# Kernel tuning notes

Measured on AMD Instinct MI355X. Metric: run time of the kernel, lower is better.

Reference implementation:

```python
import jax, jax.numpy as jnp
import numpy as np

B, S, D, H = 2, 2048, 1024, 16
HD = D // H

def setup_inputs() -> dict:
    key = jax.random.key(0)
    ks = jax.random.split(key, 9)
    scale = 1.0 / np.sqrt(D)
    return {
        "query": jax.random.normal(ks[0], (B, S, D), jnp.float32),
        "key":   jax.random.normal(ks[1], (B, S, D), jnp.float32),
        "value": jax.random.normal(ks[2], (B, S, D), jnp.float32),
        "Wq_w": jax.random.normal(ks[3], (D, D), jnp.float32) * scale,
        "Wq_b": jax.random.normal(ks[4], (D,), jnp.float32) * scale,
        "Wk_w": jax.random.normal(ks[5], (D, D), jnp.float32) * scale,
        "Wk_b": jax.random.normal(ks[6], (D,), jnp.float32) * scale,
        "Wv_w": jax.random.normal(ks[7], (D, D), jnp.float32) * scale,
        "Wv_b": jax.random.normal(ks[8], (D,), jnp.float32) * scale,
    }

def reference(query, key, value, Wq_w, Wq_b, Wk_w, Wk_b, Wv_w, Wv_b):
    b, s, d = query.shape
    # torch Linear: y = x @ W.T + b
    Q = query @ Wq_w.T + Wq_b
    K = key   @ Wk_w.T + Wk_b
    V = value @ Wv_w.T + Wv_b
    # [B, H, S, HD]
    Q = Q.reshape(b, -1, H, HD).transpose(0, 2, 1, 3)
    K = K.reshape(b, -1, H, HD).transpose(0, 2, 1, 3)
    V = V.reshape(b, -1, H, HD).transpose(0, 2, 1, 3)
    scores = jnp.einsum("bhqd,bhkd->bhqk", Q, K) / jnp.sqrt(jnp.float32(HD))
    attn = jax.nn.softmax(scores, axis=-1)
    context = jnp.einsum("bhqk,bhkd->bhqd", attn, V)  # [B,H,S,HD]
    attn_output = context.transpose(0, 2, 1, 3).reshape(b, -1, H * HD)  # [B,S,D]
    return (context, attn_output)
```

## Files before the change

### kernel.cpp

```cpp
#include <hip/hip_runtime.h>
#include <hip/hip_bf16.h>

constexpr int Bb = 2, Ss = 2048, Dd = 1024, Hh = 16, HD = 64;
constexpr int Mrows = Bb * Ss;
constexpr float QSCALE = 0.125f * 1.44269504088896f;
constexpr size_t CTX_ELEMS = (size_t)Bb * Hh * Ss * HD;

typedef __attribute__((ext_vector_type(8))) short   short8;
typedef __attribute__((ext_vector_type(4))) float   floatx4;
typedef __attribute__((ext_vector_type(8))) __bf16  bf16x8;

#define DEVI __device__ __forceinline__

DEVI unsigned short f2bf(float f) {
  union { float f; unsigned u; } x; x.f = f;
  return (unsigned short)((x.u + 0x7fffu + ((x.u >> 16) & 1u)) >> 16);
}
DEVI float fexp2(float x) {
#if __has_builtin(__builtin_amdgcn_exp2f)
  return __builtin_amdgcn_exp2f(x);
#else
  return __expf(x * 0.6931471805599453f);
#endif
}

constexpr size_t XE = (size_t)Mrows * Dd;
constexpr size_t WE = (size_t)Dd * Dd;
constexpr size_t OFF_W = 3 * XE;
constexpr size_t OFF_O = 3 * XE + 3 * WE;
constexpr size_t WS_NEED = (OFF_O + 3 * XE) * 2;

__global__ __launch_bounds__(256) void convert_bf16(
    const float* __restrict__ q, const float* __restrict__ k, const float* __restrict__ v,
    const float* __restrict__ wq, const float* __restrict__ wk, const float* __restrict__ wv,
    unsigned short* __restrict__ dst)
{
  const int sel = blockIdx.y;
  const float* src; size_t n, off;
  switch (sel) {
    case 0:  src = q;  n = XE; off = 0;            break;
    case 1:  src = k;  n = XE; off = XE;           break;
    case 2:  src = v;  n = XE; off = 2 * XE;       break;
    case 3:  src = wq; n = WE; off = OFF_W;        break;
    case 4:  src = wk; n = WE; off = OFF_W + WE;   break;
    default: src = wv; n = WE; off = OFF_W + 2*WE; break;
  }
  unsigned short* d = dst + off;
  const size_t stride = (size_t)gridDim.x * blockDim.x;
  for (size_t i = (size_t)blockIdx.x * blockDim.x + threadIdx.x; i < n / 8; i += stride) {
    const floatx4 a = *(const floatx4*)(src + i * 8);
    const floatx4 b = *(const floatx4*)(src + i * 8 + 4);
    short8 o;
    #pragma unroll
    for (int j = 0; j < 4; ++j) { o[j] = (short)f2bf(a[j]); o[4 + j] = (short)f2bf(b[j]); }
    *(short8*)(d + i * 8) = o;
  }
}

template<bool SWAP>
DEVI void store_out(floatx4 (&acc)[4][4], const float* __restrict__ bias,
                    unsigned short* __restrict__ out, float oscale,
                    int bm, int bn, int wm, int wn, int lrow, int lg)
{
  if constexpr (!SWAP) {
    #pragma unroll
    for (int ni = 0; ni < 4; ++ni) {
      const int gcol = bn * 128 + wn + ni * 16 + lrow;
      const float bval = bias[gcol];
      const int h = gcol >> 6, hd = gcol & 63;
      #pragma unroll
      for (int mi = 0; mi < 4; ++mi)
        #pragma unroll
        for (int r = 0; r < 4; ++r) {
          const int grow = bm * 128 + wm + mi * 16 + lg * 4 + r;
          const int b = grow >> 11, s = grow & 2047;
          out[(((size_t)(b * Hh + h) * Ss + s) << 6) + hd] = f2bf((acc[mi][ni][r] + bval) * oscale);
        }
    }
  } else {
    #pragma unroll
    for (int ni = 0; ni < 4; ++ni)
      #pragma unroll
      for (int r = 0; r < 4; ++r) {
        const int n = bn * 128 + wn + ni * 16 + lg * 4 + r;
        const float bval = bias[n];
        #pragma unroll
        for (int mi = 0; mi < 4; ++mi) {
          const int m = bm * 128 + wm + mi * 16 + lrow;
          out[(size_t)n * Mrows + m] = f2bf(acc[mi][ni][r] + bval);
        }
      }
  }
}

DEVI void gload16(const unsigned short* g, unsigned short* l) {
  __builtin_amdgcn_global_load_lds(
      (const __attribute__((address_space(1))) unsigned int*)g,
      (__attribute__((address_space(3))) unsigned int*)l, 16, 0, 0);
}

template<bool SWAP>
DEVI void gemm_core_bf16(const unsigned short* __restrict__ X,
                         const unsigned short* __restrict__ W,
                         const float* __restrict__ bias,
                         unsigned short* __restrict__ out, float oscale,
                         unsigned short* As, unsigned short* Bs, int bm, int bn)
{
  const int t = threadIdx.x, wid = t >> 6, lane = t & 63;
  const int lrow = lane & 15, lg = lane >> 4;
  const int wm = (wid >> 1) * 64, wn = (wid & 1) * 64;

  const int srow = lane >> 3;
  const int gch  = (lane & 7) ^ srow;
  const unsigned short* gA = X + (size_t)(bm * 128 + wid * 32 + srow) * Dd + gch * 8;
  const unsigned short* gB = W + (size_t)(bn * 128 + wid * 32 + srow) * Dd + gch * 8;
  unsigned short* lA = As + wid * 4 * 512;
  unsigned short* lB = Bs + wid * 4 * 512;

  floatx4 acc[4][4];
  #pragma unroll
  for (int i = 0; i < 4; ++i)
    #pragma unroll
    for (int j = 0; j < 4; ++j) acc[i][j] = 0.0f;

  for (int k0 = 0; k0 < Dd; k0 += 64) {
    __syncthreads();
    #pragma unroll
    for (int j = 0; j < 4; ++j) {
      gload16(gA + (size_t)j * 8 * Dd + k0, lA + j * 512);
      gload16(gB + (size_t)j * 8 * Dd + k0, lB + j * 512);
    }
    __syncthreads();

    #pragma unroll
    for (int kf = 0; kf < 2; ++kf) {
      bf16x8 af[4], bf[4];
      #pragma unroll
      for (int mi = 0; mi < 4; ++mi) {
        const int row = wm + mi * 16 + lrow;
        const int ch  = ((kf << 2) | lg) ^ (lrow & 7);
        af[mi] = __builtin_bit_cast(bf16x8, *(const short8*)&As[row * 64 + (ch << 3)]);
      }
      #pragma unroll
      for (int ni = 0; ni < 4; ++ni) {
        const int row = wn + ni * 16 + lrow;
        const int ch  = ((kf << 2) | lg) ^ (lrow & 7);
        bf[ni] = __builtin_bit_cast(bf16x8, *(const short8*)&Bs[row * 64 + (ch << 3)]);
      }
      #pragma unroll
      for (int mi = 0; mi < 4; ++mi)
        #pragma unroll
        for (int ni = 0; ni < 4; ++ni) {
          if constexpr (SWAP)
            acc[mi][ni] = __builtin_amdgcn_mfma_f32_16x16x32_bf16(bf[ni], af[mi], acc[mi][ni], 0, 0, 0);
          else
            acc[mi][ni] = __builtin_amdgcn_mfma_f32_16x16x32_bf16(af[mi], bf[ni], acc[mi][ni], 0, 0, 0);
        }
    }
  }
  store_out<SWAP>(acc, bias, out, oscale, bm, bn, wm, wn, lrow, lg);
}

__global__ __launch_bounds__(256, 3) void qkv_gemm_bf16(
    const unsigned short* __restrict__ ws,
    const float* __restrict__ bq, const float* __restrict__ bk, const float* __restrict__ bv,
    unsigned short* __restrict__ outbase)
{
  __shared__ __align__(16) unsigned short As[128 * 64];
  __shared__ __align__(16) unsigned short Bs[128 * 64];

  const int id  = blockIdx.y * 256 + blockIdx.x;
  const int swz = (id & 7) * 96 + (id >> 3);
  const int sel = swz >> 8;
  const int bx  = swz & 255;
  const int bm = bx >> 3, bn = bx & 7;

  const unsigned short* X = ws + (size_t)sel * XE;
  const unsigned short* W = ws + OFF_W + (size_t)sel * WE;
  const float* bias = sel == 0 ? bq : sel == 1 ? bk : bv;
  unsigned short* out = outbase + (size_t)sel * XE;

  if (sel == 2) gemm_core_bf16<true >(X, W, bias, out, 1.0f,   As, Bs, bm, bn);
  else          gemm_core_bf16<false>(X, W, bias, out, sel == 0 ? QSCALE : 1.0f, As, Bs, bm, bn);
}

constexpr int APAD = 40;

template<bool SWAP>
DEVI void gemm_core_f32(const float* __restrict__ X, const float* __restrict__ W,
                        const float* __restrict__ bias, unsigned short* __restrict__ out,
                        float oscale, unsigned short* As, unsigned short* Bs, int bm, int bn)
{
  const int t = threadIdx.x, wid = t >> 6, lane = t & 63;
  const int lrow = lane & 15, lg = lane >> 4;
  const int wm = (wid >> 1) * 64, wn = (wid & 1) * 64;

  floatx4 acc[4][4];
  #pragma unroll
  for (int i = 0; i < 4; ++i)
    #pragma unroll
    for (int j = 0; j < 4; ++j) acc[i][j] = 0.0f;

  for (int k0 = 0; k0 < Dd; k0 += 32) {
    __syncthreads();
    #pragma unroll
    for (int half = 0; half < 2; ++half) {
      const int cidx = t + half * 256;
      const int r = cidx >> 2, c = cidx & 3;
      {
        const float* ga = X + (size_t)(bm * 128 + r) * Dd + k0 + c * 8;
        const floatx4 x0 = *(const floatx4*)ga;
        const floatx4 x1 = *(const floatx4*)(ga + 4);
        short8 va;
        #pragma unroll
        for (int j = 0; j < 4; ++j) { va[j] = (short)f2bf(x0[j]); va[4+j] = (short)f2bf(x1[j]); }
        *(short8*)&As[r * APAD + c * 8] = va;
      }
      {
        const float* gb = W + (size_t)(bn * 128 + r) * Dd + k0 + c * 8;
        const floatx4 x0 = *(const floatx4*)gb;
        const floatx4 x1 = *(const floatx4*)(gb + 4);
        short8 vb;
        #pragma unroll
        for (int j = 0; j < 4; ++j) { vb[j] = (short)f2bf(x0[j]); vb[4+j] = (short)f2bf(x1[j]); }
        *(short8*)&Bs[r * APAD + c * 8] = vb;
      }
    }
    __syncthreads();

    bf16x8 af[4], bf[4];
    #pragma unroll
    for (int mi = 0; mi < 4; ++mi)
      af[mi] = __builtin_bit_cast(bf16x8, *(const short8*)&As[(wm + mi * 16 + lrow) * APAD + lg * 8]);
    #pragma unroll
    for (int ni = 0; ni < 4; ++ni)
      bf[ni] = __builtin_bit_cast(bf16x8, *(const short8*)&Bs[(wn + ni * 16 + lrow) * APAD + lg * 8]);

    #pragma unroll
    for (int mi = 0; mi < 4; ++mi)
      #pragma unroll
      for (int ni = 0; ni < 4; ++ni) {
        if constexpr (SWAP)
          acc[mi][ni] = __builtin_amdgcn_mfma_f32_16x16x32_bf16(bf[ni], af[mi], acc[mi][ni], 0, 0, 0);
        else
          acc[mi][ni] = __builtin_amdgcn_mfma_f32_16x16x32_bf16(af[mi], bf[ni], acc[mi][ni], 0, 0, 0);
      }
  }
  store_out<SWAP>(acc, bias, out, oscale, bm, bn, wm, wn, lrow, lg);
}

__global__ __launch_bounds__(256, 2) void qkv_gemm_f32(
    const float* __restrict__ q, const float* __restrict__ k, const float* __restrict__ v,
    const float* __restrict__ wq, const float* __restrict__ wk, const float* __restrict__ wv,
    const float* __restrict__ bq, const float* __restrict__ bk, const float* __restrict__ bv,
    unsigned short* __restrict__ outbase)
{
  __shared__ __align__(16) unsigned short As[128 * APAD];
  __shared__ __align__(16) unsigned short Bs[128 * APAD];

  const int id  = blockIdx.y * 256 + blockIdx.x;
  const int swz = (id & 7) * 96 + (id >> 3);
  const int sel = swz >> 8;
  const int bx  = swz & 255;
  const int bm = bx >> 3, bn = bx & 7;

  const float* X = sel == 0 ? q : sel == 1 ? k : v;
  const float* W = sel == 0 ? wq : sel == 1 ? wk : wv;
  const float* bias = sel == 0 ? bq : sel == 1 ? bk : bv;
  unsigned short* out = outbase + (size_t)sel * XE;

  if (sel == 2) gemm_core_f32<true >(X, W, bias, out, 1.0f, As, Bs, bm, bn);
  else          gemm_core_f32<false>(X, W, bias, out, sel == 0 ? QSCALE : 1.0f, As, Bs, bm, bn);
}

constexpr int KPAD  = 72;
constexpr int PWPAD = 72;

__global__ __launch_bounds__(256, 2) void attn_fwd(
    const unsigned short* __restrict__ Qw, const unsigned short* __restrict__ Kw,
    const unsigned short* __restrict__ Vw, float* __restrict__ out)
{
  __shared__ __align__(16) unsigned short Ks[2][64 * KPAD];
  __shared__ __align__(16) unsigned short Vt[2][64 * KPAD];
  __shared__ __align__(16) unsigned short Pw[4][32 * PWPAD];

  const int id  = blockIdx.y * 16 + blockIdx.x;
  const int swz = (id & 7) * 64 + (id >> 3);
  const int qb  = swz & 15, bh = swz >> 4;
  const int b   = bh >> 4, h = bh & 15;

  const int t = threadIdx.x, wid = t >> 6, lane = t & 63;
  const int lrow = lane & 15, lg = lane >> 4;
  const unsigned short* Qb = Qw + (size_t)bh * (Ss * HD);
  const unsigned short* Kb = Kw + (size_t)bh * (Ss * HD);
  const int q0 = qb * 128 + wid * 32;

  bf16x8 qf[2][2];
  #pragma unroll
  for (int qh = 0; qh < 2; ++qh)
    #pragma unroll
    for (int kf = 0; kf < 2; ++kf)
      qf[qh][kf] = __builtin_bit_cast(bf16x8,
          *(const short8*)(Qb + (size_t)(q0 + qh * 16 + lrow) * 64 + kf * 32 + lg * 8));

  floatx4 ctx[2][4];
  floatx4 l4[2];
  #pragma unroll
  for (int qh = 0; qh < 2; ++qh) {
    l4[qh] = 0.0f;
    #pragma unroll
    for (int ni = 0; ni < 4; ++ni) ctx[qh][ni] = 0.0f;
  }
  short8 ones_s;
  #pragma unroll
  for (int j = 0; j < 8; ++j) ones_s[j] = (short)0x3F80;
  const bf16x8 ones = __builtin_bit_cast(bf16x8, ones_s);

  const int sr = t >> 2, sc = t & 3;
  const unsigned short* kgp = Kb + (size_t)sr * 64;
  const unsigned short* vgp = Vw + (size_t)(h * 64 + sr) * Mrows + b * Ss;

  short8 kreg[2], vreg[2];
  auto stage_load = [&](int kv0) {
    #pragma unroll
    for (int hf = 0; hf < 2; ++hf) {
      const int c = sc + hf * 4;
      kreg[hf] = *(const short8*)(kgp + (size_t)kv0 * 64 + c * 8);
      vreg[hf] = *(const short8*)(vgp + kv0 + c * 8);
    }
  };
  auto stage_write = [&](int buf) {
    #pragma unroll
    for (int hf = 0; hf < 2; ++hf) {
      const int c = sc + hf * 4;
      *(short8*)&Ks[buf][sr * KPAD + c * 8] = kreg[hf];
      *(short8*)&Vt[buf][sr * KPAD + c * 8] = vreg[hf];
    }
  };

  stage_load(0);
  stage_write(0);
  __syncthreads();

  unsigned short* Pme = &Pw[wid][0];

  for (int it = 0; it < Ss / 64; ++it) {
    const int cur = it & 1;
    if (it + 1 < Ss / 64) stage_load((it + 1) * 64);

    floatx4 s4[2][4];
    #pragma unroll
    for (int qh = 0; qh < 2; ++qh)
      #pragma unroll
      for (int ni = 0; ni < 4; ++ni) s4[qh][ni] = 0.0f;
    #pragma unroll
    for (int ni = 0; ni < 4; ++ni)
      #pragma unroll
      for (int kf = 0; kf < 2; ++kf) {
        const bf16x8 kfrag = __builtin_bit_cast(bf16x8,
            *(const short8*)&Ks[cur][(ni * 16 + lrow) * KPAD + kf * 32 + lg * 8]);
        #pragma unroll
        for (int qh = 0; qh < 2; ++qh)
          s4[qh][ni] = __builtin_amdgcn_mfma_f32_16x16x32_bf16(qf[qh][kf], kfrag, s4[qh][ni], 0, 0, 0);
      }

    #pragma unroll
    for (int qh = 0; qh < 2; ++qh)
      #pragma unroll
      for (int ni = 0; ni < 4; ++ni)
        #pragma unroll
        for (int r = 0; r < 4; ++r) {
          const float p = fexp2(s4[qh][ni][r]);
          Pme[(qh * 16 + lg * 4 + r) * PWPAD + ni * 16 + lrow] = f2bf(p);
        }

    #pragma unroll
    for (int kvs = 0; kvs < 2; ++kvs) {
      bf16x8 pa[2];
      #pragma unroll
      for (int qh = 0; qh < 2; ++qh) {
        pa[qh] = __builtin_bit_cast(bf16x8,
            *(const short8*)&Pme[(qh * 16 + lrow) * PWPAD + kvs * 32 + lg * 8]);
        l4[qh] = __builtin_amdgcn_mfma_f32_16x16x32_bf16(pa[qh], ones, l4[qh], 0, 0, 0);
      }
      #pragma unroll
      for (int ni = 0; ni < 4; ++ni) {
        const bf16x8 vf = __builtin_bit_cast(bf16x8,
            *(const short8*)&Vt[cur][(ni * 16 + lrow) * KPAD + kvs * 32 + lg * 8]);
        #pragma unroll
        for (int qh = 0; qh < 2; ++qh)
          ctx[qh][ni] = __builtin_amdgcn_mfma_f32_16x16x32_bf16(pa[qh], vf, ctx[qh][ni], 0, 0, 0);
      }
    }

    if (it + 1 < Ss / 64) stage_write(cur ^ 1);
    __syncthreads();
  }

  #pragma unroll
  for (int qh = 0; qh < 2; ++qh) {
    floatx4 inv;
    #pragma unroll
    for (int r = 0; r < 4; ++r) inv[r] = 1.0f / l4[qh][r];
    #pragma unroll
    for (int ni = 0; ni < 4; ++ni) {
      const int hd = ni * 16 + lrow;
      #pragma unroll
      for (int r = 0; r < 4; ++r) {
        const int q = q0 + qh * 16 + lg * 4 + r;
        const float val = ctx[qh][ni][r] * inv[r];
        out[((size_t)bh * Ss + q) * 64 + hd] = val;
        out[CTX_ELEMS + (((size_t)(b * Ss + q)) << 10) + (h << 6) + hd] = val;
      }
    }
  }
}

extern "C" void kernel_launch(void* const* d_in, const int* in_sizes, int n_in,
                              void* d_out, int out_size, void* d_ws, size_t ws_size,
                              hipStream_t stream) {
  const float* q  = (const float*)d_in[0];
  const float* k  = (const float*)d_in[1];
  const float* v  = (const float*)d_in[2];
  const float* wq = (const float*)d_in[3];
  const float* bq = (const float*)d_in[4];
  const float* wk = (const float*)d_in[5];
  const float* bk = (const float*)d_in[6];
  const float* wv = (const float*)d_in[7];
  const float* bv = (const float*)d_in[8];
  unsigned short* ws = (unsigned short*)d_ws;
  float* out = (float*)d_out;

  if (ws_size >= WS_NEED) {
    convert_bf16<<<dim3(256, 6), 256, 0, stream>>>(q, k, v, wq, wk, wv, ws);
    qkv_gemm_bf16<<<dim3(256, 3), 256, 0, stream>>>(ws, bq, bk, bv, ws + OFF_O);
    attn_fwd<<<dim3(16, 32), 256, 0, stream>>>(ws + OFF_O, ws + OFF_O + XE, ws + OFF_O + 2 * XE, out);
  } else {
    qkv_gemm_f32<<<dim3(256, 3), 256, 0, stream>>>(q, k, v, wq, wk, wv, bq, bk, bv, ws);
    attn_fwd<<<dim3(16, 32), 256, 0, stream>>>(ws, ws + XE, ws + 2 * XE, out);
  }
}
```

Baseline: 105.4 us.

## Rewrite attention inner loop with 32x32 MFMA, register-resident P, direct LDS loads

```diff
diff --git a/kernel.cpp b/kernel.cpp
--- a/kernel.cpp
+++ b/kernel.cpp
@@ -6,9 +6,11 @@
 constexpr float QSCALE = 0.125f * 1.44269504088896f;
 constexpr size_t CTX_ELEMS = (size_t)Bb * Hh * Ss * HD;
 
-typedef __attribute__((ext_vector_type(8))) short   short8;
-typedef __attribute__((ext_vector_type(4))) float   floatx4;
-typedef __attribute__((ext_vector_type(8))) __bf16  bf16x8;
+typedef __attribute__((ext_vector_type(8)))  short        short8;
+typedef __attribute__((ext_vector_type(4)))  float        floatx4;
+typedef __attribute__((ext_vector_type(16))) float        floatx16;
+typedef __attribute__((ext_vector_type(4)))  unsigned int uintx4;
+typedef __attribute__((ext_vector_type(8)))  __bf16       bf16x8;
 
 #define DEVI __device__ __forceinline__
 
@@ -273,16 +275,12 @@
   else          gemm_core_f32<false>(X, W, bias, out, sel == 0 ? QSCALE : 1.0f, As, Bs, bm, bn);
 }
 
-constexpr int KPAD  = 72;
-constexpr int PWPAD = 72;
-
 __global__ __launch_bounds__(256, 2) void attn_fwd(
     const unsigned short* __restrict__ Qw, const unsigned short* __restrict__ Kw,
     const unsigned short* __restrict__ Vw, float* __restrict__ out)
 {
-  __shared__ __align__(16) unsigned short Ks[2][64 * KPAD];
-  __shared__ __align__(16) unsigned short Vt[2][64 * KPAD];
-  __shared__ __align__(16) unsigned short Pw[4][32 * PWPAD];
+  __shared__ __align__(16) unsigned short Ks[2][64 * 64];
+  __shared__ __align__(16) unsigned short Vt[2][64 * 64];
 
   const int id  = blockIdx.y * 16 + blockIdx.x;
   const int swz = (id & 7) * 64 + (id >> 3);
@@ -290,128 +288,104 @@
   const int b   = bh >> 4, h = bh & 15;
 
   const int t = threadIdx.x, wid = t >> 6, lane = t & 63;
-  const int lrow = lane & 15, lg = lane >> 4;
+  const int l31 = lane & 31, hi = lane >> 5;
   const unsigned short* Qb = Qw + (size_t)bh * (Ss * HD);
   const unsigned short* Kb = Kw + (size_t)bh * (Ss * HD);
+  const unsigned short* Vg = Vw + (size_t)(h * 64) * Mrows + b * Ss;
   const int q0 = qb * 128 + wid * 32;
 
-  bf16x8 qf[2][2];
-  #pragma unroll
-  for (int qh = 0; qh < 2; ++qh)
-    #pragma unroll
-    for (int kf = 0; kf < 2; ++kf)
-      qf[qh][kf] = __builtin_bit_cast(bf16x8,
-          *(const short8*)(Qb + (size_t)(q0 + qh * 16 + lrow) * 64 + kf * 32 + lg * 8));
-
-  floatx4 ctx[2][4];
-  floatx4 l4[2];
-  #pragma unroll
-  for (int qh = 0; qh < 2; ++qh) {
-    l4[qh] = 0.0f;
-    #pragma unroll
-    for (int ni = 0; ni < 4; ++ni) ctx[qh][ni] = 0.0f;
-  }
+  bf16x8 qf[4];
+  #pragma unroll
+  for (int hs = 0; hs < 4; ++hs)
+    qf[hs] = __builtin_bit_cast(bf16x8,
+        *(const short8*)(Qb + (size_t)(q0 + l31) * 64 + hs * 16 + hi * 8));
+
+  floatx16 ctx[2], lsum;
+  #pragma unroll
+  for (int nb = 0; nb < 2; ++nb) ctx[nb] = 0.0f;
+  lsum = 0.0f;
+
   short8 ones_s;
   #pragma unroll
   for (int j = 0; j < 8; ++j) ones_s[j] = (short)0x3F80;
   const bf16x8 ones = __builtin_bit_cast(bf16x8, ones_s);
 
-  const int sr = t >> 2, sc = t & 3;
-  const unsigned short* kgp = Kb + (size_t)sr * 64;
-  const unsigned short* vgp = Vw + (size_t)(h * 64 + sr) * Mrows + b * Ss;
-
-  short8 kreg[2], vreg[2];
-  auto stage_load = [&](int kv0) {
-    #pragma unroll
-    for (int hf = 0; hf < 2; ++hf) {
-      const int c = sc + hf * 4;
-      kreg[hf] = *(const short8*)(kgp + (size_t)kv0 * 64 + c * 8);
-      vreg[hf] = *(const short8*)(vgp + kv0 + c * 8);
+  const int rl = lane >> 3;
+  const int cs = (lane & 7) ^ rl;
+  auto stage = [&](int kv0, int buf) {
+    #pragma unroll
+    for (int i = 0; i < 2; ++i) {
+      const int row = wid * 16 + i * 8 + rl;
+      gload16(Kb + (size_t)(kv0 + row) * 64 + cs * 8, &Ks[buf][(wid * 16 + i * 8) * 64]);
+      gload16(Vg + (size_t)row * Mrows + kv0 + cs * 8, &Vt[buf][(wid * 16 + i * 8) * 64]);
     }
   };
-  auto stage_write = [&](int buf) {
-    #pragma unroll
-    for (int hf = 0; hf < 2; ++hf) {
-      const int c = sc + hf * 4;
-      *(short8*)&Ks[buf][sr * KPAD + c * 8] = kreg[hf];
-      *(short8*)&Vt[buf][sr * KPAD + c * 8] = vreg[hf];
-    }
-  };
-
-  stage_load(0);
-  stage_write(0);
-  __syncthreads();
-
-  unsigned short* Pme = &Pw[wid][0];
+
+  stage(0, 0);
 
   for (int it = 0; it < Ss / 64; ++it) {
     const int cur = it & 1;
-    if (it + 1 < Ss / 64) stage_load((it + 1) * 64);
-
-    floatx4 s4[2][4];
-    #pragma unroll
-    for (int qh = 0; qh < 2; ++qh)
-      #pragma unroll
-      for (int ni = 0; ni < 4; ++ni) s4[qh][ni] = 0.0f;
-    #pragma unroll
-    for (int ni = 0; ni < 4; ++ni)
-      #pragma unroll
-      for (int kf = 0; kf < 2; ++kf) {
-        const bf16x8 kfrag = __builtin_bit_cast(bf16x8,
-            *(const short8*)&Ks[cur][(ni * 16 + lrow) * KPAD + kf * 32 + lg * 8]);
-        #pragma unroll
-        for (int qh = 0; qh < 2; ++qh)
-          s4[qh][ni] = __builtin_amdgcn_mfma_f32_16x16x32_bf16(qf[qh][kf], kfrag, s4[qh][ni], 0, 0, 0);
-      }
-
-    #pragma unroll
-    for (int qh = 0; qh < 2; ++qh)
-      #pragma unroll
-      for (int ni = 0; ni < 4; ++ni)
-        #pragma unroll
-        for (int r = 0; r < 4; ++r) {
-          const float p = fexp2(s4[qh][ni][r]);
-          Pme[(qh * 16 + lg * 4 + r) * PWPAD + ni * 16 + lrow] = f2bf(p);
+    __syncthreads();
+    if (it + 1 < Ss / 64) stage((it + 1) * 64, cur ^ 1);
+
+    floatx16 s[2];
+    s[0] = 0.0f; s[1] = 0.0f;
+    __builtin_amdgcn_s_setprio(1);
+    #pragma unroll
+    for (int kvb = 0; kvb < 2; ++kvb)
+      #pragma unroll
+      for (int hs = 0; hs < 4; ++hs) {
+        const int ch = ((hs << 1) | hi) ^ (l31 & 7);
+        const bf16x8 kf = __builtin_bit_cast(bf16x8,
+            *(const short8*)&Ks[cur][(kvb * 32 + l31) * 64 + (ch << 3)]);
+        s[kvb] = __builtin_amdgcn_mfma_f32_32x32x16_bf16(kf, qf[hs], s[kvb], 0, 0, 0);
+      }
+    __builtin_amdgcn_s_setprio(0);
+
+    #pragma unroll
+    for (int kvb = 0; kvb < 2; ++kvb) {
+      float p[16];
+      #pragma unroll
+      for (int r = 0; r < 16; ++r) p[r] = fexp2(s[kvb][r]);
+      unsigned int c[8];
+      #pragma unroll
+      for (int i = 0; i < 8; ++i)
+        asm("v_cvt_pk_bf16_f32 %0, %1, %2" : "=v"(c[i]) : "v"(p[2 * i]), "v"(p[2 * i + 1]));
+
+      #pragma unroll
+      for (int ks2 = 0; ks2 < 2; ++ks2) {
+        unsigned int w0 = c[4 * ks2 + 0], w2 = c[4 * ks2 + 2];
+        unsigned int w1 = c[4 * ks2 + 1], w3 = c[4 * ks2 + 3];
+        asm("v_permlane32_swap_b32 %0, %1" : "+v"(w0), "+v"(w2));
+        asm("v_permlane32_swap_b32 %0, %1" : "+v"(w1), "+v"(w3));
+        uintx4 paw; paw[0] = w0; paw[1] = w1; paw[2] = w2; paw[3] = w3;
+        const bf16x8 pa = __builtin_bit_cast(bf16x8, paw);
+
+        const int ks = kvb * 2 + ks2;
+        __builtin_amdgcn_s_setprio(1);
+        lsum = __builtin_amdgcn_mfma_f32_32x32x16_bf16(pa, ones, lsum, 0, 0, 0);
+        #pragma unroll
+        for (int nb = 0; nb < 2; ++nb) {
+          const int ch = ((ks << 1) | hi) ^ (l31 & 7);
+          const bf16x8 vf = __builtin_bit_cast(bf16x8,
+              *(const short8*)&Vt[cur][(nb * 32 + l31) * 64 + (ch << 3)]);
+          ctx[nb] = __builtin_amdgcn_mfma_f32_32x32x16_bf16(pa, vf, ctx[nb], 0, 0, 0);
         }
-
-    #pragma unroll
-    for (int kvs = 0; kvs < 2; ++kvs) {
-      bf16x8 pa[2];
-      #pragma unroll
-      for (int qh = 0; qh < 2; ++qh) {
-        pa[qh] = __builtin_bit_cast(bf16x8,
-            *(const short8*)&Pme[(qh * 16 + lrow) * PWPAD + kvs * 32 + lg * 8]);
-        l4[qh] = __builtin_amdgcn_mfma_f32_16x16x32_bf16(pa[qh], ones, l4[qh], 0, 0, 0);
-      }
-      #pragma unroll
-      for (int ni = 0; ni < 4; ++ni) {
-        const bf16x8 vf = __builtin_bit_cast(bf16x8,
-            *(const short8*)&Vt[cur][(ni * 16 + lrow) * KPAD + kvs * 32 + lg * 8]);
-        #pragma unroll
-        for (int qh = 0; qh < 2; ++qh)
-          ctx[qh][ni] = __builtin_amdgcn_mfma_f32_16x16x32_bf16(pa[qh], vf, ctx[qh][ni], 0, 0, 0);
-      }
-    }
-
-    if (it + 1 < Ss / 64) stage_write(cur ^ 1);
-    __syncthreads();
-  }
-
-  #pragma unroll
-  for (int qh = 0; qh < 2; ++qh) {
-    floatx4 inv;
-    #pragma unroll
-    for (int r = 0; r < 4; ++r) inv[r] = 1.0f / l4[qh][r];
-    #pragma unroll
-    for (int ni = 0; ni < 4; ++ni) {
-      const int hd = ni * 16 + lrow;
-      #pragma unroll
-      for (int r = 0; r < 4; ++r) {
-        const int q = q0 + qh * 16 + lg * 4 + r;
-        const float val = ctx[qh][ni][r] * inv[r];
-        out[((size_t)bh * Ss + q) * 64 + hd] = val;
-        out[CTX_ELEMS + (((size_t)(b * Ss + q)) << 10) + (h << 6) + hd] = val;
-      }
+        __builtin_amdgcn_s_setprio(0);
+      }
+    }
+  }
+
+  #pragma unroll
+  for (int r = 0; r < 16; ++r) {
+    const float inv = 1.0f / lsum[r];
+    const int qrow = q0 + (r & 3) + 8 * (r >> 2) + 4 * hi;
+    #pragma unroll
+    for (int nb = 0; nb < 2; ++nb) {
+      const int hd = nb * 32 + l31;
+      const float val = ctx[nb][r] * inv;
+      out[((size_t)bh * Ss + qrow) * 64 + hd] = val;
+      out[CTX_ELEMS + (((size_t)(b * Ss + qrow)) << 10) + (h << 6) + hd] = val;
     }
   }
 }
```

After: 92.97 us. 11.8% less time.
